# Performance work log

Hardware: AMD Instinct MI355X
Metric: run time of the kernel (lower is better)

Reference implementation:

```python
import jax, jax.numpy as jnp
import numpy as np

B, D, H, NG = 8192, 2048, 2048, 7  # batch, input_size, hidden_size, num gate networks


def setup_inputs() -> dict:
    key = jax.random.key(0)
    ks = jax.random.split(key, 7)
    hx = jax.random.normal(ks[0], (B, D), dtype=jnp.float32)
    cx1 = jax.random.normal(ks[1], (B, H), dtype=jnp.float32)
    cx2 = jax.random.normal(ks[2], (B, H), dtype=jnp.float32)
    tj = jax.random.uniform(ks[3], (B, 1), dtype=jnp.float32)
    dt = jax.random.uniform(ks[4], (B, 1), dtype=jnp.float32)
    # fused weights for the 7 gate/decay networks, order: i1,i2,f1,f2,o,z,d
    W = jax.random.normal(ks[5], (D, NG * H), dtype=jnp.float32) * (1.0 / np.sqrt(D))
    b = jax.random.normal(ks[6], (NG * H,), dtype=jnp.float32) * 0.01
    return {"hx": hx, "cx1": cx1, "cx2": cx2, "tj": tj, "dt": dt, "W": W, "b": b}


def reference(hx, cx1, cx2, tj, dt, W, b):
    # One fused GEMM for all 7 gate networks, then split.
    g = hx @ W + b  # [B, 7H]
    i1, i2, f1, f2, o, z_raw, d_raw = [g[:, k * H:(k + 1) * H] for k in range(NG)]
    sig = jax.nn.sigmoid
    i1, i2, f1, f2, o = sig(i1), sig(i2), sig(f1), sig(f2), sig(o)
    z = jnp.tanh(z_raw)                 # Tanh(LC_z(hx)) as in forward
    decay = jax.nn.softplus(d_raw)      # Decay_network: positive decay coeff
    cy1 = f1 * cx1 + i1 * z             # fast cell state
    cy2 = f2 * cx2 + i2 * z             # asymptotic cell state
    t = tj + dt
    # continuous-time decay: c(t) = cy2 + (cy1 - cy2) * exp(-decay * (t - tj))
    c_t = cy2 + (cy1 - cy2) * jnp.exp(-decay * (t - tj))
    h_t = o * jnp.tanh(c_t)             # get_h(t)
    return jnp.stack([cy1, cy2, h_t])   # [3, B, H]
```

## Files before the change

kernel.cpp:

```cpp
#include <hip/hip_runtime.h>
#include <hip/hip_bf16.h>
#include <stdint.h>


#define B_SZ 8192
#define D_SZ 2048
#define H_SZ 2048
#define NG   7
#define NW   (NG * H_SZ)
#define BM   256
#define BN   32
#define BK   32
#define NKST (D_SZ / BK)
#define NBX  (B_SZ / BM)
#define NBY  (H_SZ / BN)

#define WB_BYTES   ((size_t)NBY * NKST * 14336)
#define HXB_OFF    WB_BYTES
#define HXB_BYTES  ((size_t)NBX * NKST * 16384)
#define WS_NEEDED  (WB_BYTES + HXB_BYTES)

typedef __attribute__((ext_vector_type(8))) short bf16x8;
typedef __attribute__((ext_vector_type(4))) float f32x4;

__device__ __forceinline__ uint32_t cvtpk(float lo, float hi) {
    uint32_t r;
    asm("v_cvt_pk_bf16_f32 %0, %1, %2" : "=v"(r) : "v"(lo), "v"(hi));
    return r;
}
__device__ __forceinline__ void glds16(const void* g, void* l) {
    __builtin_amdgcn_global_load_lds(
        (const __attribute__((address_space(1))) uint32_t*)g,
        (__attribute__((address_space(3))) uint32_t*)l, 16, 0, 0);
}
__device__ __forceinline__ float sigmoidf_(float x) {
    return 1.0f / (1.0f + __expf(-x));
}
__device__ __forceinline__ float tanhf_(float x) {
    float ax = fabsf(x);
    float e = __expf(2.0f * ax);
    float t = 1.0f - 2.0f / (e + 1.0f);
    return copysignf(t, x);
}
__device__ __forceinline__ float softplusf_(float x) {
    return (x > 30.0f) ? x : __logf(1.0f + __expf(x));
}

__global__ __launch_bounds__(896) void conv_w(const float* __restrict__ W,
                                              char* __restrict__ wb)
{
    const int by = blockIdx.x >> 6;
    const int ks = blockIdx.x & 63;
    const int u  = threadIdx.x;
    const int r  = u >> 2;
    const int pc = u & 3;
    const int koct = pc ^ ((r >> 1) & 3);
    const int g  = r >> 5;
    const int n  = r & 31;
    const int col = g * H_SZ + by * BN + n;
    const float* src = W + (size_t)(ks * BK + koct * 8) * NW + col;
    float w0 = src[0];
    float w1 = src[(size_t)NW];
    float w2 = src[(size_t)2 * NW];
    float w3 = src[(size_t)3 * NW];
    float w4 = src[(size_t)4 * NW];
    float w5 = src[(size_t)5 * NW];
    float w6 = src[(size_t)6 * NW];
    float w7 = src[(size_t)7 * NW];
    uint4 o;
    o.x = cvtpk(w0, w1); o.y = cvtpk(w2, w3);
    o.z = cvtpk(w4, w5); o.w = cvtpk(w6, w7);
    *(uint4*)(wb + (size_t)blockIdx.x * 14336 + u * 16) = o;
}

__global__ __launch_bounds__(1024) void conv_hx(const float* __restrict__ hx,
                                                char* __restrict__ hxb)
{
    const int bx = blockIdx.x >> 6;
    const int ks = blockIdx.x & 63;
    const int u  = threadIdx.x;
    const int r  = u >> 2;
    const int pc = u & 3;
    const int koct = pc ^ ((r >> 1) & 3);
    const float* src = hx + (size_t)(bx * BM + r) * D_SZ + ks * BK + koct * 8;
    f32x4 a = *(const f32x4*)(src);
    f32x4 b = *(const f32x4*)(src + 4);
    uint4 o;
    o.x = cvtpk(a[0], a[1]); o.y = cvtpk(a[2], a[3]);
    o.z = cvtpk(b[0], b[1]); o.w = cvtpk(b[2], b[3]);
    *(uint4*)(hxb + (size_t)blockIdx.x * 16384 + u * 16) = o;
}

#define NTH3 1024
__global__ __launch_bounds__(NTH3, 4) void lstm_bf16(
    const char* __restrict__ wb, const char* __restrict__ hxb,
    const float* __restrict__ cx1, const float* __restrict__ cx2,
    const float* __restrict__ dt, const float* __restrict__ bias,
    float* __restrict__ out)
{
    __shared__ char smem[2 * 16384 + 2 * 14336];

    const int tid  = threadIdx.x;
    const int lane = tid & 63;
    const int wid  = tid >> 6;
    const int wm   = wid >> 1;
    const int wn   = wid & 1;
    const int l15  = lane & 15;
    const int lg   = lane >> 4;

    const int b0  = blockIdx.x;
    const int swz = (b0 & 7) * 256 + (b0 >> 3);
    const int by2 = swz >> 6;
    const int rem = swz & 63;
    const int bx  = rem >> 1;
    const int by  = by2 * 2 + (rem & 1);
    const int gm0 = bx * BM;
    const int n0  = by * BN;

    const size_t hx_tile0 = (size_t)(bx * NKST) << 14;
    const size_t w_tile0  = (size_t)(by * NKST) * 14336;

    const int xch  = (lg ^ ((l15 >> 1) & 3)) * 8;
    const int aoff0 = (wm * 32 + l15) * 32 + xch;
    const int aoff1 = aoff0 + 16 * 32;
    int boff[NG];
    #pragma unroll
    for (int g = 0; g < NG; ++g)
        boff[g] = (g * 32 + wn * 16 + l15) * 32 + xch;

    f32x4 acc[NG][2];
    #pragma unroll
    for (int g = 0; g < NG; ++g) {
        acc[g][0] = (f32x4){0.f, 0.f, 0.f, 0.f};
        acc[g][1] = (f32x4){0.f, 0.f, 0.f, 0.f};
    }

    const int lane16 = lane << 4;

    auto stage = [&](int c, int k) {
        {
            const char* src = hxb + hx_tile0 + ((size_t)k << 14) + (wid << 10) + lane16;
            glds16(src, smem + c * 16384 + (wid << 10));
        }
        if (wid < 14) {
            const char* src = wb + w_tile0 + (size_t)k * 14336 + (wid << 10) + lane16;
            glds16(src, smem + 2 * 16384 + c * 14336 + (wid << 10));
        }
    };

    auto compute = [&](int c) {
        const ushort* sa = (const ushort*)(smem + c * 16384);
        const ushort* sb = (const ushort*)(smem + 2 * 16384 + c * 14336);
        bf16x8 af0 = *(const bf16x8*)(sa + aoff0);
        bf16x8 af1 = *(const bf16x8*)(sa + aoff1);
        #pragma unroll
        for (int g = 0; g < NG; ++g) {
            bf16x8 bfr = *(const bf16x8*)(sb + boff[g]);
            acc[g][0] = __builtin_amdgcn_mfma_f32_16x16x32_bf16(af0, bfr, acc[g][0], 0, 0, 0);
            acc[g][1] = __builtin_amdgcn_mfma_f32_16x16x32_bf16(af1, bfr, acc[g][1], 0, 0, 0);
        }
    };

    stage(0, 0);
    __syncthreads();
    for (int k = 0; k < NKST; k += 2) {
        stage(1, k + 1);
        compute(0);
        __syncthreads();
        if (k + 2 < NKST) stage(0, k + 2);
        compute(1);
        __syncthreads();
    }

    const size_t BH = (size_t)B_SZ * H_SZ;
    const int j = n0 + wn * 16 + l15;
    float bj[NG];
    #pragma unroll
    for (int g = 0; g < NG; ++g) bj[g] = bias[g * H_SZ + j];

    #pragma unroll
    for (int mf = 0; mf < 2; ++mf) {
        #pragma unroll
        for (int r = 0; r < 4; ++r) {
            int row = gm0 + wm * 32 + mf * 16 + lg * 4 + r;
            float dtv = dt[row];
            float i1 = sigmoidf_(acc[0][mf][r] + bj[0]);
            float i2 = sigmoidf_(acc[1][mf][r] + bj[1]);
            float f1 = sigmoidf_(acc[2][mf][r] + bj[2]);
            float f2 = sigmoidf_(acc[3][mf][r] + bj[3]);
            float o  = sigmoidf_(acc[4][mf][r] + bj[4]);
            float z  = tanhf_(acc[5][mf][r] + bj[5]);
            float dec = softplusf_(acc[6][mf][r] + bj[6]);
            size_t idx = (size_t)row * H_SZ + j;
            float c1 = cx1[idx], c2 = cx2[idx];
            float cy1 = f1 * c1 + i1 * z;
            float cy2 = f2 * c2 + i2 * z;
            float ct  = cy2 + (cy1 - cy2) * __expf(-dec * dtv);
            float ht  = o * tanhf_(ct);
            out[idx]          = cy1;
            out[BH + idx]     = cy2;
            out[2 * BH + idx] = ht;
        }
    }
}

#define NTH  512
#define LDP  40
__global__ __launch_bounds__(NTH, 2) void lstm_f32(
    const float* __restrict__ hx, const float* __restrict__ cx1,
    const float* __restrict__ cx2, const float* __restrict__ dt,
    const float* __restrict__ W, const float* __restrict__ bias,
    float* __restrict__ out)
{
    __shared__ ushort sA[BM * LDP];
    __shared__ ushort sB[NG * BN * LDP];

    const int tid = threadIdx.x;
    const int nwg = gridDim.x;
    const int cpx = nwg >> 3;
    const int b0  = blockIdx.x;
    const int swz = (b0 & 7) * cpx + (b0 >> 3);
    const int bx  = swz & 31;
    const int by  = swz >> 5;
    const int gm0 = bx * BM;
    const int n0  = by * BN;

    const int lane = tid & 63;
    const int wid  = tid >> 6;
    const int wm   = wid >> 1;
    const int wn   = wid & 1;
    const int l15  = lane & 15;
    const int lg   = lane >> 4;

    const int ar0 = tid >> 2,          aq0 = tid & 3;
    const int ar1 = (tid + 512) >> 2,  aq1 = tid & 3;
    const bool hasB = (tid < 448);
    const int bg  = tid >> 6;
    const int bkq = (tid >> 3) & 7;
    const int bnq = tid & 7;

    f32x4 pa[4];
    f32x4 pb[4];

    auto issue_loads = [&](int K0) {
        {
            const float* p = hx + (size_t)(gm0 + ar0) * D_SZ + K0 + aq0 * 8;
            pa[0] = *(const f32x4*)(p);
            pa[1] = *(const f32x4*)(p + 4);
        }
        {
            const float* p = hx + (size_t)(gm0 + ar1) * D_SZ + K0 + aq1 * 8;
            pa[2] = *(const f32x4*)(p);
            pa[3] = *(const f32x4*)(p + 4);
        }
        if (hasB) {
            const float* p = W + (size_t)(K0 + bkq * 4) * NW + bg * H_SZ + n0 + bnq * 4;
            pb[0] = *(const f32x4*)(p);
            pb[1] = *(const f32x4*)(p + NW);
            pb[2] = *(const f32x4*)(p + 2 * NW);
            pb[3] = *(const f32x4*)(p + 3 * NW);
        }
    };

    auto store_lds = [&]() {
        {
            uint4 u;
            u.x = cvtpk(pa[0][0], pa[0][1]); u.y = cvtpk(pa[0][2], pa[0][3]);
            u.z = cvtpk(pa[1][0], pa[1][1]); u.w = cvtpk(pa[1][2], pa[1][3]);
            *(uint4*)(&sA[ar0 * LDP + aq0 * 8]) = u;
        }
        {
            uint4 u;
            u.x = cvtpk(pa[2][0], pa[2][1]); u.y = cvtpk(pa[2][2], pa[2][3]);
            u.z = cvtpk(pa[3][0], pa[3][1]); u.w = cvtpk(pa[3][2], pa[3][3]);
            *(uint4*)(&sA[ar1 * LDP + aq1 * 8]) = u;
        }
        if (hasB) {
            #pragma unroll
            for (int jj = 0; jj < 4; ++jj) {
                uint2 v;
                v.x = cvtpk(pb[0][jj], pb[1][jj]);
                v.y = cvtpk(pb[2][jj], pb[3][jj]);
                *(uint2*)(&sB[(bg * BN + bnq * 4 + jj) * LDP + bkq * 4]) = v;
            }
        }
    };

    f32x4 acc[NG][4];
    #pragma unroll
    for (int g = 0; g < NG; ++g)
        #pragma unroll
        for (int mf = 0; mf < 4; ++mf)
            acc[g][mf] = (f32x4){0.f, 0.f, 0.f, 0.f};

    int aoff[4];
    #pragma unroll
    for (int mf = 0; mf < 4; ++mf)
        aoff[mf] = (wm * 64 + mf * 16 + l15) * LDP + lg * 8;
    int boff[NG];
    #pragma unroll
    for (int g = 0; g < NG; ++g)
        boff[g] = (g * BN + wn * 16 + l15) * LDP + lg * 8;

    issue_loads(0);
    for (int kk = 0; kk < NKST; ++kk) {
        store_lds();
        __syncthreads();
        if (kk + 1 < NKST) issue_loads((kk + 1) * BK);

        bf16x8 af[4];
        #pragma unroll
        for (int mf = 0; mf < 4; ++mf)
            af[mf] = *(const bf16x8*)(&sA[aoff[mf]]);
        #pragma unroll
        for (int g = 0; g < NG; ++g) {
            bf16x8 bfr = *(const bf16x8*)(&sB[boff[g]]);
            #pragma unroll
            for (int mf = 0; mf < 4; ++mf)
                acc[g][mf] = __builtin_amdgcn_mfma_f32_16x16x32_bf16(
                    af[mf], bfr, acc[g][mf], 0, 0, 0);
        }
        __syncthreads();
    }

    const size_t BH = (size_t)B_SZ * H_SZ;
    const int j = n0 + wn * 16 + l15;
    float bj[NG];
    #pragma unroll
    for (int g = 0; g < NG; ++g) bj[g] = bias[g * H_SZ + j];

    #pragma unroll
    for (int mf = 0; mf < 4; ++mf) {
        #pragma unroll
        for (int r = 0; r < 4; ++r) {
            int row = gm0 + wm * 64 + mf * 16 + lg * 4 + r;
            float dtv = dt[row];
            float i1 = sigmoidf_(acc[0][mf][r] + bj[0]);
            float i2 = sigmoidf_(acc[1][mf][r] + bj[1]);
            float f1 = sigmoidf_(acc[2][mf][r] + bj[2]);
            float f2 = sigmoidf_(acc[3][mf][r] + bj[3]);
            float o  = sigmoidf_(acc[4][mf][r] + bj[4]);
            float z  = tanhf_(acc[5][mf][r] + bj[5]);
            float dec = softplusf_(acc[6][mf][r] + bj[6]);
            size_t idx = (size_t)row * H_SZ + j;
            float c1 = cx1[idx], c2 = cx2[idx];
            float cy1 = f1 * c1 + i1 * z;
            float cy2 = f2 * c2 + i2 * z;
            float ct  = cy2 + (cy1 - cy2) * __expf(-dec * dtv);
            float ht  = o * tanhf_(ct);
            out[idx]          = cy1;
            out[BH + idx]     = cy2;
            out[2 * BH + idx] = ht;
        }
    }
}

extern "C" void kernel_launch(void* const* d_in, const int* in_sizes, int n_in,
                              void* d_out, int out_size, void* d_ws, size_t ws_size,
                              hipStream_t stream) {
    const float* hx  = (const float*)d_in[0];
    const float* cx1 = (const float*)d_in[1];
    const float* cx2 = (const float*)d_in[2];
    const float* dt  = (const float*)d_in[4];
    const float* W   = (const float*)d_in[5];
    const float* b   = (const float*)d_in[6];
    float* out = (float*)d_out;

    if (ws_size >= WS_NEEDED) {
        char* wb  = (char*)d_ws;
        char* hxb = (char*)d_ws + HXB_OFF;
        conv_w<<<dim3(NBY * NKST), dim3(896), 0, stream>>>(W, wb);
        conv_hx<<<dim3(NBX * NKST), dim3(1024), 0, stream>>>(hx, hxb);
        lstm_bf16<<<dim3(NBX * NBY), dim3(NTH3), 0, stream>>>(
            wb, hxb, cx1, cx2, dt, b, out);
    } else {
        lstm_f32<<<dim3(NBX * NBY), dim3(NTH), 0, stream>>>(
            hx, cx1, cx2, dt, W, b, out);
    }
}
```

Baseline: 548.0 us.

## Use four-stage LDS pipeline with vmcnt waits instead of double buffering

Replaces the two-buffer stage/compute loop with a four-buffer ring that keeps three k-tiles of global-to-LDS loads in flight. A single barrier per iteration, preceded by a partial s_waitcnt vmcnt, replaces the full __syncthreads pairs. The weight-tile load is also redistributed so all 16 waves each load 896 bytes (56 lanes) instead of 14 waves loading 1KB. This roughly doubles LDS use (120KB per block), which may limit occupancy, and the correctness of the hand-tuned vmcnt counts depends on each lane issuing exactly two loads per stage.

```diff
diff --git a/kernel.cpp b/kernel.cpp
--- a/kernel.cpp
+++ b/kernel.cpp
@@ -92,13 +92,21 @@
 }
 
 #define NTH3 1024
+#define BUFB 30720
+#define NBUF 4
+
+#define PIPE_WAIT(N)                                        \
+    asm volatile("s_waitcnt vmcnt(" #N ")" ::: "memory");   \
+    __builtin_amdgcn_s_barrier();                           \
+    asm volatile("" ::: "memory");
+
 __global__ __launch_bounds__(NTH3, 4) void lstm_bf16(
     const char* __restrict__ wb, const char* __restrict__ hxb,
     const float* __restrict__ cx1, const float* __restrict__ cx2,
     const float* __restrict__ dt, const float* __restrict__ bias,
     float* __restrict__ out)
 {
-    __shared__ char smem[2 * 16384 + 2 * 14336];
+    __shared__ char smem[NBUF * BUFB];
 
     const int tid  = threadIdx.x;
     const int lane = tid & 63;
@@ -140,17 +148,17 @@
     auto stage = [&](int c, int k) {
         {
             const char* src = hxb + hx_tile0 + ((size_t)k << 14) + (wid << 10) + lane16;
-            glds16(src, smem + c * 16384 + (wid << 10));
-        }
-        if (wid < 14) {
-            const char* src = wb + w_tile0 + (size_t)k * 14336 + (wid << 10) + lane16;
-            glds16(src, smem + 2 * 16384 + c * 14336 + (wid << 10));
+            glds16(src, smem + c * BUFB + (wid << 10));
+        }
+        if (lane < 56) {
+            const char* src = wb + w_tile0 + (size_t)k * 14336 + wid * 896 + lane16;
+            glds16(src, smem + c * BUFB + 16384 + wid * 896);
         }
     };
 
     auto compute = [&](int c) {
-        const ushort* sa = (const ushort*)(smem + c * 16384);
-        const ushort* sb = (const ushort*)(smem + 2 * 16384 + c * 14336);
+        const ushort* sa = (const ushort*)(smem + c * BUFB);
+        const ushort* sb = (const ushort*)(smem + c * BUFB + 16384);
         bf16x8 af0 = *(const bf16x8*)(sa + aoff0);
         bf16x8 af1 = *(const bf16x8*)(sa + aoff1);
         #pragma unroll
@@ -162,15 +170,20 @@
     };
 
     stage(0, 0);
-    __syncthreads();
-    for (int k = 0; k < NKST; k += 2) {
-        stage(1, k + 1);
-        compute(0);
-        __syncthreads();
-        if (k + 2 < NKST) stage(0, k + 2);
-        compute(1);
-        __syncthreads();
-    }
+    stage(1, 1);
+    stage(2, 2);
+
+    for (int t = 0; t < NKST - 3; ++t) {
+        PIPE_WAIT(4)
+        stage((t + 3) & 3, t + 3);
+        compute(t & 3);
+    }
+    PIPE_WAIT(4)
+    compute((NKST - 3) & 3);
+    PIPE_WAIT(2)
+    compute((NKST - 2) & 3);
+    PIPE_WAIT(0)
+    compute((NKST - 1) & 3);
 
     const size_t BH = (size_t)B_SZ * H_SZ;
     const int j = n0 + wn * 16 + l15;
```

Measured after the change: 543.9 us. About the same (-0.8%).

## Restructure bf16 GEMM into 4-stage LDS pipeline with 512 threads and register double-buffering

Applied to the files above, without the earlier changes.

Rewrites the main bf16 LSTM kernel's GEMM mainloop. It drops from 1024 to 512 threads per block, so each wave now computes 64 rows, and it uses a 4-deep LDS ring buffer filled by direct global-to-LDS loads. LDS fragments are double-buffered in registers with inline-asm ds_read, and vmcnt/lgkmcnt waits plus a single s_barrier replace the full __syncthreads pairs. The MFMA clusters run at raised wave priority. The aim is to hide global and LDS latency behind the matrix-core work, at the cost of more registers and LDS per block (lower occupancy) and fragile hand-tuned wait counts.

```diff
diff --git a/kernel.cpp b/kernel.cpp
--- a/kernel.cpp
+++ b/kernel.cpp
@@ -91,14 +91,26 @@
     *(uint4*)(hxb + (size_t)blockIdx.x * 16384 + u * 16) = o;
 }
 
-#define NTH3 1024
-__global__ __launch_bounds__(NTH3, 4) void lstm_bf16(
+#define NTH3 512
+#define BUFB 30720
+#define NBUF 4
+
+#define SB0 __builtin_amdgcn_sched_barrier(0)
+#define WAIT_LGKM0 do {                                          \
+    asm volatile("s_waitcnt lgkmcnt(0)" ::: "memory");           \
+    SB0; } while (0)
+#define WAIT_VM(N) do {                                          \
+    asm volatile("s_waitcnt vmcnt(" #N ")" ::: "memory");        \
+    __builtin_amdgcn_s_barrier();                                \
+    SB0; } while (0)
+
+__global__ __launch_bounds__(NTH3, 2) void lstm_bf16(
     const char* __restrict__ wb, const char* __restrict__ hxb,
     const float* __restrict__ cx1, const float* __restrict__ cx2,
     const float* __restrict__ dt, const float* __restrict__ bias,
     float* __restrict__ out)
 {
-    __shared__ char smem[2 * 16384 + 2 * 14336];
+    __shared__ char smem[NBUF * BUFB];
 
     const int tid  = threadIdx.x;
     const int lane = tid & 63;
@@ -120,171 +132,21 @@
     const size_t hx_tile0 = (size_t)(bx * NKST) << 14;
     const size_t w_tile0  = (size_t)(by * NKST) * 14336;
 
-    const int xch  = (lg ^ ((l15 >> 1) & 3)) * 8;
-    const int aoff0 = (wm * 32 + l15) * 32 + xch;
-    const int aoff1 = aoff0 + 16 * 32;
-    int boff[NG];
-    #pragma unroll
-    for (int g = 0; g < NG; ++g)
-        boff[g] = (g * 32 + wn * 16 + l15) * 32 + xch;
-
-    f32x4 acc[NG][2];
-    #pragma unroll
-    for (int g = 0; g < NG; ++g) {
-        acc[g][0] = (f32x4){0.f, 0.f, 0.f, 0.f};
-        acc[g][1] = (f32x4){0.f, 0.f, 0.f, 0.f};
-    }
+    const int xch = (lg ^ ((l15 >> 1) & 3)) * 8;
+    const uint32_t aAb = (uint32_t)(uintptr_t)(smem) + 2u * ((wm * 64 + l15) * 32 + xch);
+    const uint32_t aBb = (uint32_t)(uintptr_t)(smem) + 16384u + 2u * ((wn * 16 + l15) * 32 + xch);
+    const uint32_t aA0 = aAb,            aA1 = aAb + BUFB;
+    const uint32_t aA2 = aAb + 2 * BUFB, aA3 = aAb + 3 * BUFB;
+    const uint32_t aB0 = aBb,            aB1 = aBb + BUFB;
+    const uint32_t aB2 = aBb + 2 * BUFB, aB3 = aBb + 3 * BUFB;
 
     const int lane16 = lane << 4;
-
-    auto stage = [&](int c, int k) {
-        {
-            const char* src = hxb + hx_tile0 + ((size_t)k << 14) + (wid << 10) + lane16;
-            glds16(src, smem + c * 16384 + (wid << 10));
-        }
-        if (wid < 14) {
-            const char* src = wb + w_tile0 + (size_t)k * 14336 + (wid << 10) + lane16;
-            glds16(src, smem + 2 * 16384 + c * 14336 + (wid << 10));
-        }
-    };
-
-    auto compute = [&](int c) {
-        const ushort* sa = (const ushort*)(smem + c * 16384);
-        const ushort* sb = (const ushort*)(smem + 2 * 16384 + c * 14336);
-        bf16x8 af0 = *(const bf16x8*)(sa + aoff0);
-        bf16x8 af1 = *(const bf16x8*)(sa + aoff1);
-        #pragma unroll
-        for (int g = 0; g < NG; ++g) {
-            bf16x8 bfr = *(const bf16x8*)(sb + boff[g]);
-            acc[g][0] = __builtin_amdgcn_mfma_f32_16x16x32_bf16(af0, bfr, acc[g][0], 0, 0, 0);
-            acc[g][1] = __builtin_amdgcn_mfma_f32_16x16x32_bf16(af1, bfr, acc[g][1], 0, 0, 0);
-        }
-    };
-
-    stage(0, 0);
-    __syncthreads();
-    for (int k = 0; k < NKST; k += 2) {
-        stage(1, k + 1);
-        compute(0);
-        __syncthreads();
-        if (k + 2 < NKST) stage(0, k + 2);
-        compute(1);
-        __syncthreads();
-    }
-
-    const size_t BH = (size_t)B_SZ * H_SZ;
-    const int j = n0 + wn * 16 + l15;
-    float bj[NG];
-    #pragma unroll
-    for (int g = 0; g < NG; ++g) bj[g] = bias[g * H_SZ + j];
-
-    #pragma unroll
-    for (int mf = 0; mf < 2; ++mf) {
-        #pragma unroll
-        for (int r = 0; r < 4; ++r) {
-            int row = gm0 + wm * 32 + mf * 16 + lg * 4 + r;
-            float dtv = dt[row];
-            float i1 = sigmoidf_(acc[0][mf][r] + bj[0]);
-            float i2 = sigmoidf_(acc[1][mf][r] + bj[1]);
-            float f1 = sigmoidf_(acc[2][mf][r] + bj[2]);
-            float f2 = sigmoidf_(acc[3][mf][r] + bj[3]);
-            float o  = sigmoidf_(acc[4][mf][r] + bj[4]);
-            float z  = tanhf_(acc[5][mf][r] + bj[5]);
-            float dec = softplusf_(acc[6][mf][r] + bj[6]);
-            size_t idx = (size_t)row * H_SZ + j;
-            float c1 = cx1[idx], c2 = cx2[idx];
-            float cy1 = f1 * c1 + i1 * z;
-            float cy2 = f2 * c2 + i2 * z;
-            float ct  = cy2 + (cy1 - cy2) * __expf(-dec * dtv);
-            float ht  = o * tanhf_(ct);
-            out[idx]          = cy1;
-            out[BH + idx]     = cy2;
-            out[2 * BH + idx] = ht;
-        }
-    }
-}
-
-#define NTH  512
-#define LDP  40
-__global__ __launch_bounds__(NTH, 2) void lstm_f32(
-    const float* __restrict__ hx, const float* __restrict__ cx1,
-    const float* __restrict__ cx2, const float* __restrict__ dt,
-    const float* __restrict__ W, const float* __restrict__ bias,
-    float* __restrict__ out)
-{
-    __shared__ ushort sA[BM * LDP];
-    __shared__ ushort sB[NG * BN * LDP];
-
-    const int tid = threadIdx.x;
-    const int nwg = gridDim.x;
-    const int cpx = nwg >> 3;
-    const int b0  = blockIdx.x;
-    const int swz = (b0 & 7) * cpx + (b0 >> 3);
-    const int bx  = swz & 31;
-    const int by  = swz >> 5;
-    const int gm0 = bx * BM;
-    const int n0  = by * BN;
-
-    const int lane = tid & 63;
-    const int wid  = tid >> 6;
-    const int wm   = wid >> 1;
-    const int wn   = wid & 1;
-    const int l15  = lane & 15;
-    const int lg   = lane >> 4;
-
-    const int ar0 = tid >> 2,          aq0 = tid & 3;
-    const int ar1 = (tid + 512) >> 2,  aq1 = tid & 3;
-    const bool hasB = (tid < 448);
-    const int bg  = tid >> 6;
-    const int bkq = (tid >> 3) & 7;
-    const int bnq = tid & 7;
-
-    f32x4 pa[4];
-    f32x4 pb[4];
-
-    auto issue_loads = [&](int K0) {
-        {
-            const float* p = hx + (size_t)(gm0 + ar0) * D_SZ + K0 + aq0 * 8;
-            pa[0] = *(const f32x4*)(p);
-            pa[1] = *(const f32x4*)(p + 4);
-        }
-        {
-            const float* p = hx + (size_t)(gm0 + ar1) * D_SZ + K0 + aq1 * 8;
-            pa[2] = *(const f32x4*)(p);
-            pa[3] = *(const f32x4*)(p + 4);
-        }
-        if (hasB) {
-            const float* p = W + (size_t)(K0 + bkq * 4) * NW + bg * H_SZ + n0 + bnq * 4;
-            pb[0] = *(const f32x4*)(p);
-            pb[1] = *(const f32x4*)(p + NW);
-            pb[2] = *(const f32x4*)(p + 2 * NW);
-            pb[3] = *(const f32x4*)(p + 3 * NW);
-        }
-    };
-
-    auto store_lds = [&]() {
-        {
-            uint4 u;
-            u.x = cvtpk(pa[0][0], pa[0][1]); u.y = cvtpk(pa[0][2], pa[0][3]);
-            u.z = cvtpk(pa[1][0], pa[1][1]); u.w = cvtpk(pa[1][2], pa[1][3]);
-            *(uint4*)(&sA[ar0 * LDP + aq0 * 8]) = u;
-        }
-        {
-            uint4 u;
-            u.x = cvtpk(pa[2][0], pa[2][1]); u.y = cvtpk(pa[2][2], pa[2][3]);
-            u.z = cvtpk(pa[3][0], pa[3][1]); u.w = cvtpk(pa[3][2], pa[3][3]);
-            *(uint4*)(&sA[ar1 * LDP + aq1 * 8]) = u;
-        }
-        if (hasB) {
-            #pragma unroll
-            for (int jj = 0; jj < 4; ++jj) {
-                uint2 v;
-                v.x = cvtpk(pb[0][jj], pb[1][jj]);
-                v.y = cvtpk(pb[2][jj], pb[3][jj]);
-                *(uint2*)(&sB[(bg * BN + bnq * 4 + jj) * LDP + bkq * 4]) = v;
-            }
-        }
-    };
+    const char* hxp0 = hxb + hx_tile0 + (wid << 11) + lane16;
+    const char* wbp0 = wb + w_tile0 + wid * 1792 + lane16;
+    char* dA0 = smem + (wid << 11);            char* dB0 = smem + 16384 + wid * 1792;
+    char* dA1 = dA0 + BUFB;                    char* dB1 = dB0 + BUFB;
+    char* dA2 = dA0 + 2 * BUFB;                char* dB2 = dB0 + 2 * BUFB;
+    char* dA3 = dA0 + 3 * BUFB;                char* dB3 = dB0 + 3 * BUFB;
 
     f32x4 acc[NG][4];
     #pragma unroll
@@ -293,35 +155,78 @@
         for (int mf = 0; mf < 4; ++mf)
             acc[g][mf] = (f32x4){0.f, 0.f, 0.f, 0.f};
 
-    int aoff[4];
-    #pragma unroll
-    for (int mf = 0; mf < 4; ++mf)
-        aoff[mf] = (wm * 64 + mf * 16 + l15) * LDP + lg * 8;
-    int boff[NG];
-    #pragma unroll
-    for (int g = 0; g < NG; ++g)
-        boff[g] = (g * BN + wn * 16 + l15) * LDP + lg * 8;
-
-    issue_loads(0);
-    for (int kk = 0; kk < NKST; ++kk) {
-        store_lds();
-        __syncthreads();
-        if (kk + 1 < NKST) issue_loads((kk + 1) * BK);
-
-        bf16x8 af[4];
-        #pragma unroll
-        for (int mf = 0; mf < 4; ++mf)
-            af[mf] = *(const bf16x8*)(&sA[aoff[mf]]);
-        #pragma unroll
-        for (int g = 0; g < NG; ++g) {
-            bf16x8 bfr = *(const bf16x8*)(&sB[boff[g]]);
-            #pragma unroll
-            for (int mf = 0; mf < 4; ++mf)
-                acc[g][mf] = __builtin_amdgcn_mfma_f32_16x16x32_bf16(
-                    af[mf], bfr, acc[g][mf], 0, 0, 0);
-        }
-        __syncthreads();
+    bf16x8 fA[2][4];
+    bf16x8 fB[2][7];
+
+    #define ISSUE_FRAGS(S, AA, AB) do {                                           \
+        asm volatile("s_mov_b32 m0, -1" ::);                                      \
+        asm volatile("ds_read_b128 %0, %1"                : "=v"(fA[S][0]) : "v"(AA)); \
+        asm volatile("ds_read_b128 %0, %1 offset:1024"    : "=v"(fA[S][1]) : "v"(AA)); \
+        asm volatile("ds_read_b128 %0, %1 offset:2048"    : "=v"(fA[S][2]) : "v"(AA)); \
+        asm volatile("ds_read_b128 %0, %1 offset:3072"    : "=v"(fA[S][3]) : "v"(AA)); \
+        asm volatile("ds_read_b128 %0, %1"                : "=v"(fB[S][0]) : "v"(AB)); \
+        asm volatile("ds_read_b128 %0, %1 offset:2048"    : "=v"(fB[S][1]) : "v"(AB)); \
+        asm volatile("ds_read_b128 %0, %1 offset:4096"    : "=v"(fB[S][2]) : "v"(AB)); \
+        asm volatile("ds_read_b128 %0, %1 offset:6144"    : "=v"(fB[S][3]) : "v"(AB)); \
+        asm volatile("ds_read_b128 %0, %1 offset:8192"    : "=v"(fB[S][4]) : "v"(AB)); \
+        asm volatile("ds_read_b128 %0, %1 offset:10240"   : "=v"(fB[S][5]) : "v"(AB)); \
+        asm volatile("ds_read_b128 %0, %1 offset:12288"   : "=v"(fB[S][6]) : "v"(AB)); \
+        SB0; } while (0)
+
+    #define CLUSTER(S) do {                                                       \
+        __builtin_amdgcn_s_setprio(1);                                            \
+        _Pragma("unroll")                                                         \
+        for (int g_ = 0; g_ < NG; ++g_)                                           \
+            _Pragma("unroll")                                                     \
+            for (int mf_ = 0; mf_ < 4; ++mf_)                                     \
+                acc[g_][mf_] = __builtin_amdgcn_mfma_f32_16x16x32_bf16(           \
+                    fA[S][mf_], fB[S][g_], acc[g_][mf_], 0, 0, 0);                \
+        __builtin_amdgcn_s_setprio(0);                                            \
+        SB0; } while (0)
+
+    #define STAGE_C(c) do {                                                       \
+        glds16(hxp, dA##c); glds16(hxp + 1024, dA##c + 1024);                     \
+        glds16(wbp, dB##c);                                                       \
+        if (lane < 48) glds16(wbp + 1024, dB##c + 1024);                          \
+        hxp += 16384; wbp += 14336; } while (0)
+
+    #define STAGE_K(c, k) do {                                                    \
+        glds16(hxp0 + (k) * 16384, dA##c);                                        \
+        glds16(hxp0 + (k) * 16384 + 1024, dA##c + 1024);                          \
+        glds16(wbp0 + (k) * 14336, dB##c);                                        \
+        if (lane < 48) glds16(wbp0 + (k) * 14336 + 1024, dB##c + 1024);           \
+    } while (0)
+
+    #define K_STEP(CN, SCUR, SNXT, VMN, STG) do {                                 \
+        WAIT_LGKM0;                 \
+        WAIT_VM(VMN);               \
+        ISSUE_FRAGS(SNXT, aA##CN, aB##CN);                                        \
+        STG;                                                                      \
+        SB0;                                                                      \
+        CLUSTER(SCUR); } while (0)
+
+    STAGE_K(0, 0);
+    STAGE_K(1, 1);
+    STAGE_K(2, 2);
+    const char* hxp = hxp0 + 3 * 16384;
+    const char* wbp = wbp0 + 3 * 14336;
+    asm volatile("s_waitcnt vmcnt(8)" ::: "memory");
+    __builtin_amdgcn_s_barrier();
+    SB0;
+    ISSUE_FRAGS(0, aA0, aB0);
+
+    #pragma unroll 1
+    for (int it = 0; it < 15; ++it) {
+        K_STEP(1, 0, 1, 4, STAGE_C(3));
+        K_STEP(2, 1, 0, 4, STAGE_C(0));
+        K_STEP(3, 0, 1, 4, STAGE_C(1));
+        K_STEP(0, 1, 0, 4, STAGE_C(2));
     }
+    K_STEP(1, 0, 1, 4, STAGE_C(3));
+    K_STEP(2, 1, 0, 4, (void)0);
+    K_STEP(3, 0, 1, 0, (void)0);
+    WAIT_LGKM0;
+    CLUSTER(1);
 
     const size_t BH = (size_t)B_SZ * H_SZ;
     const int j = n0 + wn * 16 + l15;
@@ -355,6 +260,157 @@
     }
 }
 
+#define NTH  512
+#define LDP  40
+__global__ __launch_bounds__(NTH, 2) void lstm_f32(
+    const float* __restrict__ hx, const float* __restrict__ cx1,
+    const float* __restrict__ cx2, const float* __restrict__ dt,
+    const float* __restrict__ W, const float* __restrict__ bias,
+    float* __restrict__ out)
+{
+    __shared__ ushort sA[BM * LDP];
+    __shared__ ushort sB[NG * BN * LDP];
+
+    const int tid = threadIdx.x;
+    const int nwg = gridDim.x;
+    const int cpx = nwg >> 3;
+    const int b0  = blockIdx.x;
+    const int swz = (b0 & 7) * cpx + (b0 >> 3);
+    const int bx  = swz & 31;
+    const int by  = swz >> 5;
+    const int gm0 = bx * BM;
+    const int n0  = by * BN;
+
+    const int lane = tid & 63;
+    const int wid  = tid >> 6;
+    const int wm   = wid >> 1;
+    const int wn   = wid & 1;
+    const int l15  = lane & 15;
+    const int lg   = lane >> 4;
+
+    const int ar0 = tid >> 2,          aq0 = tid & 3;
+    const int ar1 = (tid + 512) >> 2,  aq1 = tid & 3;
+    const bool hasB = (tid < 448);
+    const int bg  = tid >> 6;
+    const int bkq = (tid >> 3) & 7;
+    const int bnq = tid & 7;
+
+    f32x4 pa[4];
+    f32x4 pb[4];
+
+    auto issue_loads = [&](int K0) {
+        {
+            const float* p = hx + (size_t)(gm0 + ar0) * D_SZ + K0 + aq0 * 8;
+            pa[0] = *(const f32x4*)(p);
+            pa[1] = *(const f32x4*)(p + 4);
+        }
+        {
+            const float* p = hx + (size_t)(gm0 + ar1) * D_SZ + K0 + aq1 * 8;
+            pa[2] = *(const f32x4*)(p);
+            pa[3] = *(const f32x4*)(p + 4);
+        }
+        if (hasB) {
+            const float* p = W + (size_t)(K0 + bkq * 4) * NW + bg * H_SZ + n0 + bnq * 4;
+            pb[0] = *(const f32x4*)(p);
+            pb[1] = *(const f32x4*)(p + NW);
+            pb[2] = *(const f32x4*)(p + 2 * NW);
+            pb[3] = *(const f32x4*)(p + 3 * NW);
+        }
+    };
+
+    auto store_lds = [&]() {
+        {
+            uint4 u;
+            u.x = cvtpk(pa[0][0], pa[0][1]); u.y = cvtpk(pa[0][2], pa[0][3]);
+            u.z = cvtpk(pa[1][0], pa[1][1]); u.w = cvtpk(pa[1][2], pa[1][3]);
+            *(uint4*)(&sA[ar0 * LDP + aq0 * 8]) = u;
+        }
+        {
+            uint4 u;
+            u.x = cvtpk(pa[2][0], pa[2][1]); u.y = cvtpk(pa[2][2], pa[2][3]);
+            u.z = cvtpk(pa[3][0], pa[3][1]); u.w = cvtpk(pa[3][2], pa[3][3]);
+            *(uint4*)(&sA[ar1 * LDP + aq1 * 8]) = u;
+        }
+        if (hasB) {
+            #pragma unroll
+            for (int jj = 0; jj < 4; ++jj) {
+                uint2 v;
+                v.x = cvtpk(pb[0][jj], pb[1][jj]);
+                v.y = cvtpk(pb[2][jj], pb[3][jj]);
+                *(uint2*)(&sB[(bg * BN + bnq * 4 + jj) * LDP + bkq * 4]) = v;
+            }
+        }
+    };
+
+    f32x4 acc[NG][4];
+    #pragma unroll
+    for (int g = 0; g < NG; ++g)
+        #pragma unroll
+        for (int mf = 0; mf < 4; ++mf)
+            acc[g][mf] = (f32x4){0.f, 0.f, 0.f, 0.f};
+
+    int aoff[4];
+    #pragma unroll
+    for (int mf = 0; mf < 4; ++mf)
+        aoff[mf] = (wm * 64 + mf * 16 + l15) * LDP + lg * 8;
+    int boff[NG];
+    #pragma unroll
+    for (int g = 0; g < NG; ++g)
+        boff[g] = (g * BN + wn * 16 + l15) * LDP + lg * 8;
+
+    issue_loads(0);
+    for (int kk = 0; kk < NKST; ++kk) {
+        store_lds();
+        __syncthreads();
+        if (kk + 1 < NKST) issue_loads((kk + 1) * BK);
+
+        bf16x8 af[4];
+        #pragma unroll
+        for (int mf = 0; mf < 4; ++mf)
+            af[mf] = *(const bf16x8*)(&sA[aoff[mf]]);
+        #pragma unroll
+        for (int g = 0; g < NG; ++g) {
+            bf16x8 bfr = *(const bf16x8*)(&sB[boff[g]]);
+            #pragma unroll
+            for (int mf = 0; mf < 4; ++mf)
+                acc[g][mf] = __builtin_amdgcn_mfma_f32_16x16x32_bf16(
+                    af[mf], bfr, acc[g][mf], 0, 0, 0);
+        }
+        __syncthreads();
+    }
+
+    const size_t BH = (size_t)B_SZ * H_SZ;
+    const int j = n0 + wn * 16 + l15;
+    float bj[NG];
+    #pragma unroll
+    for (int g = 0; g < NG; ++g) bj[g] = bias[g * H_SZ + j];
+
+    #pragma unroll
+    for (int mf = 0; mf < 4; ++mf) {
+        #pragma unroll
+        for (int r = 0; r < 4; ++r) {
+            int row = gm0 + wm * 64 + mf * 16 + lg * 4 + r;
+            float dtv = dt[row];
+            float i1 = sigmoidf_(acc[0][mf][r] + bj[0]);
+            float i2 = sigmoidf_(acc[1][mf][r] + bj[1]);
+            float f1 = sigmoidf_(acc[2][mf][r] + bj[2]);
+            float f2 = sigmoidf_(acc[3][mf][r] + bj[3]);
+            float o  = sigmoidf_(acc[4][mf][r] + bj[4]);
+            float z  = tanhf_(acc[5][mf][r] + bj[5]);
+            float dec = softplusf_(acc[6][mf][r] + bj[6]);
+            size_t idx = (size_t)row * H_SZ + j;
+            float c1 = cx1[idx], c2 = cx2[idx];
+            float cy1 = f1 * c1 + i1 * z;
+            float cy2 = f2 * c2 + i2 * z;
+            float ct  = cy2 + (cy1 - cy2) * __expf(-dec * dtv);
+            float ht  = o * tanhf_(ct);
+            out[idx]          = cy1;
+            out[BH + idx]     = cy2;
+            out[2 * BH + idx] = ht;
+        }
+    }
+}
+
 extern "C" void kernel_launch(void* const* d_in, const int* in_sizes, int n_in,
                               void* d_out, int out_size, void* d_ws, size_t ws_size,
                               hipStream_t stream) {
```

After: 612.1 us. +11.7%, slower.

## Read A fragments directly from global and triple-buffer weight tiles in LDS

Applied to the files above, without the earlier changes.

The bf16 GEMM kernel no longer stages the hx tile through LDS. Each wave loads its A fragments straight from the pre-converted global buffer, whose layout is now unswizzled so lanes read contiguous rows. Only the weight tile is staged, using a three-deep LDS ring with one barrier per k-step, explicit vmcnt waits, sched barriers and setprio around the MFMAs. The aim is to cut LDS traffic and barrier count and raise occupancy through a smaller LDS footprint. The cost is that every wave issues redundant global A reads that must hit in cache.

```diff
diff --git a/kernel.cpp b/kernel.cpp
--- a/kernel.cpp
+++ b/kernel.cpp
@@ -81,8 +81,7 @@
     const int u  = threadIdx.x;
     const int r  = u >> 2;
     const int pc = u & 3;
-    const int koct = pc ^ ((r >> 1) & 3);
-    const float* src = hx + (size_t)(bx * BM + r) * D_SZ + ks * BK + koct * 8;
+    const float* src = hx + (size_t)(bx * BM + r) * D_SZ + ks * BK + pc * 8;
     f32x4 a = *(const f32x4*)(src);
     f32x4 b = *(const f32x4*)(src + 4);
     uint4 o;
@@ -92,13 +91,18 @@
 }
 
 #define NTH3 1024
+#define BUFB 14336
+#define NBUF 3
+
+#define SB0 __builtin_amdgcn_sched_barrier(0)
+
 __global__ __launch_bounds__(NTH3, 4) void lstm_bf16(
     const char* __restrict__ wb, const char* __restrict__ hxb,
     const float* __restrict__ cx1, const float* __restrict__ cx2,
     const float* __restrict__ dt, const float* __restrict__ bias,
     float* __restrict__ out)
 {
-    __shared__ char smem[2 * 16384 + 2 * 14336];
+    __shared__ char smem[NBUF * BUFB];
 
     const int tid  = threadIdx.x;
     const int lane = tid & 63;
@@ -117,16 +121,14 @@
     const int gm0 = bx * BM;
     const int n0  = by * BN;
 
-    const size_t hx_tile0 = (size_t)(bx * NKST) << 14;
-    const size_t w_tile0  = (size_t)(by * NKST) * 14336;
-
-    const int xch  = (lg ^ ((l15 >> 1) & 3)) * 8;
-    const int aoff0 = (wm * 32 + l15) * 32 + xch;
-    const int aoff1 = aoff0 + 16 * 32;
-    int boff[NG];
-    #pragma unroll
-    for (int g = 0; g < NG; ++g)
-        boff[g] = (g * 32 + wn * 16 + l15) * 32 + xch;
+    const char* pa = hxb + ((size_t)(bx * NKST) << 14)
+                   + (wm * 32 + l15) * 64 + lg * 16;
+    const char* wbase = wb + (size_t)(by * NKST) * 14336;
+    const int stG = (wid << 10) + (lane << 4);
+    const int stL = (wid << 10);
+    const char* pw = wbase + 2 * 14336 + stG;
+
+    const int boffu = (wn * 16 + l15) * 32 + (lg ^ ((l15 >> 1) & 3)) * 8;
 
     f32x4 acc[NG][2];
     #pragma unroll
@@ -135,42 +137,48 @@
         acc[g][1] = (f32x4){0.f, 0.f, 0.f, 0.f};
     }
 
-    const int lane16 = lane << 4;
-
-    auto stage = [&](int c, int k) {
-        {
-            const char* src = hxb + hx_tile0 + ((size_t)k << 14) + (wid << 10) + lane16;
-            glds16(src, smem + c * 16384 + (wid << 10));
-        }
-        if (wid < 14) {
-            const char* src = wb + w_tile0 + (size_t)k * 14336 + (wid << 10) + lane16;
-            glds16(src, smem + 2 * 16384 + c * 14336 + (wid << 10));
-        }
-    };
-
-    auto compute = [&](int c) {
-        const ushort* sa = (const ushort*)(smem + c * 16384);
-        const ushort* sb = (const ushort*)(smem + 2 * 16384 + c * 14336);
-        bf16x8 af0 = *(const bf16x8*)(sa + aoff0);
-        bf16x8 af1 = *(const bf16x8*)(sa + aoff1);
-        #pragma unroll
-        for (int g = 0; g < NG; ++g) {
-            bf16x8 bfr = *(const bf16x8*)(sb + boff[g]);
-            acc[g][0] = __builtin_amdgcn_mfma_f32_16x16x32_bf16(af0, bfr, acc[g][0], 0, 0, 0);
-            acc[g][1] = __builtin_amdgcn_mfma_f32_16x16x32_bf16(af1, bfr, acc[g][1], 0, 0, 0);
-        }
-    };
-
-    stage(0, 0);
-    __syncthreads();
-    for (int k = 0; k < NKST; k += 2) {
-        stage(1, k + 1);
-        compute(0);
-        __syncthreads();
-        if (k + 2 < NKST) stage(0, k + 2);
-        compute(1);
-        __syncthreads();
-    }
+    if (wid < 14) {
+        glds16(wbase + stG, smem + stL);
+        glds16(wbase + 14336 + stG, smem + BUFB + stL);
+    }
+
+    #define BODY(CUR, NXT, VMN, STG) do {                                      \
+        asm volatile("s_waitcnt vmcnt(" #VMN ")" ::: "memory");                \
+        __builtin_amdgcn_s_barrier();                                          \
+        SB0;                                                                   \
+        bf16x8 bfr[NG];                                                        \
+        const ushort* sb_ = (const ushort*)(smem + (CUR) * BUFB) + boffu;      \
+        _Pragma("unroll")                                                      \
+        for (int g_ = 0; g_ < NG; ++g_)                                        \
+            bfr[g_] = *(const bf16x8*)(sb_ + g_ * 1024);                       \
+        bf16x8 a0_ = *(const bf16x8*)(pa);                                     \
+        bf16x8 a1_ = *(const bf16x8*)(pa + 1024);                              \
+        SB0;                                                                   \
+        if ((STG) && wid < 14) glds16(pw, smem + (NXT) * BUFB + stL);          \
+        SB0;                                                                   \
+        __builtin_amdgcn_s_setprio(1);                                         \
+        _Pragma("unroll")                                                      \
+        for (int g_ = 0; g_ < NG; ++g_) {                                      \
+            acc[g_][0] = __builtin_amdgcn_mfma_f32_16x16x32_bf16(              \
+                a0_, bfr[g_], acc[g_][0], 0, 0, 0);                            \
+            acc[g_][1] = __builtin_amdgcn_mfma_f32_16x16x32_bf16(              \
+                a1_, bfr[g_], acc[g_][1], 0, 0, 0);                            \
+        }                                                                      \
+        __builtin_amdgcn_s_setprio(0);                                         \
+        SB0;                                                                   \
+        pa += 16384; pw += 14336;                                              \
+    } while (0)
+
+    #pragma unroll 1
+    for (int it = 0; it < 20; ++it) {
+        BODY(0, 2, 1, 1);
+        BODY(1, 0, 1, 1);
+        BODY(2, 1, 1, 1);
+    }
+    BODY(0, 2, 1, 1);
+    BODY(1, 0, 1, 1);
+    BODY(2, 1, 1, 0);
+    BODY(0, 0, 0, 0);
 
     const size_t BH = (size_t)B_SZ * H_SZ;
     const int j = n0 + wn * 16 + l15;
@@ -202,6 +210,7 @@
             out[2 * BH + idx] = ht;
         }
     }
+    #undef BODY
 }
 
 #define NTH  512
```

After: 647.1 us. +18.1%, slower.
